# Kernel optimization log

Hardware: AMD Instinct MI355X
Metric: run time of the kernel (lower is better)

## Reference

```python
import jax, jax.numpy as jnp
import numpy as np

N_MODELS = 64
IN_F = 256
OUT_F = 256
BATCH = 8192


def setup_inputs() -> dict:
    key = jax.random.key(0)
    kx, kw, kb, ki = jax.random.split(key, 4)
    x = jax.random.normal(kx, (BATCH, OUT_F), dtype=jnp.float32)
    idxs = jax.random.randint(ki, (BATCH,), 0, N_MODELS, dtype=jnp.int64)
    # learned parameters (torch inits them to zeros; we use random so grads/outputs are nontrivial)
    w = jax.random.normal(kw, (N_MODELS, IN_F, OUT_F), dtype=jnp.float32) * 0.02
    b = jax.random.normal(kb, (N_MODELS, OUT_F), dtype=jnp.float32) * 0.02
    return {"x": x, "idxs": idxs, "w": w, "b": b}


def reference(x, idxs, w, b):
    # torch: baddbmm(b[idxs,:,None], w[idxs], x[:,:,None]).squeeze(-1) -> relu
    # y[n, i] = b[idxs[n], i] + sum_o w[idxs[n], i, o] * x[n, o]
    wg = w[idxs]                      # (B, in, out) gathered per-sample weights
    bg = b[idxs]                      # (B, out)
    y = jnp.einsum('bio,bo->bi', wg, x) + bg
    return jax.nn.relu(y)
```

## Files before the change

### kernel.cpp

```cpp
#include <hip/hip_runtime.h>
#include <stdint.h>


#define N_MODELS 64
#define IN_F     256
#define OUT_F    256
#define BATCH    8192
#define BM       128
#define BN       128

typedef __bf16 bf16x8 __attribute__((ext_vector_type(8)));
typedef float  f32x4  __attribute__((ext_vector_type(4)));
typedef __attribute__((address_space(3))) uint32_t lds_u32;
typedef const __attribute__((address_space(1))) uint32_t glb_u32;

__device__ __forceinline__ void dma16(const void* g, void* l) {
  __builtin_amdgcn_global_load_lds((glb_u32*)g, (lds_u32*)l, 16, 0, 0);
}

__device__ __forceinline__ void barrier_lds_only() {
  asm volatile("s_waitcnt lgkmcnt(0)" ::: "memory");
  __builtin_amdgcn_s_barrier();
  __builtin_amdgcn_sched_barrier(0);
}

__device__ __forceinline__ bf16x8 pack8(float4 a, float4 b) {
  bf16x8 o;
  o[0] = (__bf16)a.x; o[1] = (__bf16)a.y; o[2] = (__bf16)a.z; o[3] = (__bf16)a.w;
  o[4] = (__bf16)b.x; o[5] = (__bf16)b.y; o[6] = (__bf16)b.z; o[7] = (__bf16)b.w;
  return o;
}

__global__ __launch_bounds__(1024) void fused_kernel(
    const float* __restrict__ x, const int* __restrict__ idxs,
    const float* __restrict__ w, const float* __restrict__ bias_g,
    float* __restrict__ out) {
  const int b     = (blockIdx.x & 7) * 32 + (blockIdx.x >> 3);
  const int model = b >> 2;
  const int s     = (b >> 1) & 1;
  const int i0    = (b & 1) * BN;
  const int t     = threadIdx.x;
  const int lane  = t & 63;
  const int wv    = t >> 6;

  __shared__ float w_lds[2][BM][64];
  __shared__ float x_lds[2][BM][64];
  __shared__ int rid[BM];
  __shared__ int wsum[16];

  const float* wbase = w + (size_t)model * (IN_F * OUT_F) + (size_t)i0 * IN_F;
  const int l_r = lane >> 4;
  const int l_c = lane & 15;
#define W_DMA(q, buf)                                                        \
  {                                                                          \
    _Pragma("unroll")                                                        \
    for (int j = 0; j < 2; ++j) {                                            \
      const int r0 = wv * 8 + j * 4;                                         \
      const int rr = r0 + l_r;                                               \
      const float* gs = wbase + (size_t)rr * IN_F + (q) * 64                 \
                        + ((l_c ^ (rr & 7)) << 2);                           \
      dma16(gs, &w_lds[buf][r0][0]);                                         \
    }                                                                        \
  }

  const int4* ip = (const int4*)idxs + t * 2;
  int4 iv0 = ip[0], iv1 = ip[1];

  if (s == 0) { W_DMA(0, 0) W_DMA(1, 1) }

  if (t < BM) rid[t] = -1;

  int cnt = (iv0.x == model) + (iv0.y == model) + (iv0.z == model) + (iv0.w == model)
          + (iv1.x == model) + (iv1.y == model) + (iv1.z == model) + (iv1.w == model);
  int inc = cnt;
#pragma unroll
  for (int d = 1; d < 64; d <<= 1) {
    int u = __shfl_up(inc, d);
    if (lane >= d) inc += u;
  }
  if (lane == 63) wsum[wv] = inc;
  barrier_lds_only();
  int wpre = 0, total = 0;
#pragma unroll
  for (int j = 0; j < 16; ++j) {
    int sj = wsum[j];
    total += sj;
    if (j < wv) wpre += sj;
  }
  const int start = s * BM;
  if (start >= total) return;
  if (s == 1) { W_DMA(0, 0) W_DMA(1, 1) }

  int off = wpre + inc - cnt - start;
  {
    int n0 = t * 8;
    if (iv0.x == model) { if ((unsigned)off < BM) rid[off] = n0 + 0; ++off; }
    if (iv0.y == model) { if ((unsigned)off < BM) rid[off] = n0 + 1; ++off; }
    if (iv0.z == model) { if ((unsigned)off < BM) rid[off] = n0 + 2; ++off; }
    if (iv0.w == model) { if ((unsigned)off < BM) rid[off] = n0 + 3; ++off; }
    if (iv1.x == model) { if ((unsigned)off < BM) rid[off] = n0 + 4; ++off; }
    if (iv1.y == model) { if ((unsigned)off < BM) rid[off] = n0 + 5; ++off; }
    if (iv1.z == model) { if ((unsigned)off < BM) rid[off] = n0 + 6; ++off; }
    if (iv1.w == model) { if ((unsigned)off < BM) rid[off] = n0 + 7; ++off; }
  }
  barrier_lds_only();

  const int   r_0 = wv * 4 + l_r;
  const int   r_1 = 64 + wv * 4 + l_r;
  const int   sr0 = rid[r_0];
  const int   sr1 = rid[r_1];
  const float* xb0 = x + (size_t)(sr0 < 0 ? 0 : sr0) * IN_F
                       + ((l_c ^ (r_0 & 7)) << 2);
  const float* xb1 = x + (size_t)(sr1 < 0 ? 0 : sr1) * IN_F
                       + ((l_c ^ (r_1 & 7)) << 2);
#define X_DMA(q, buf)                                                        \
  {                                                                          \
    dma16(xb0 + (q) * 64, &x_lds[buf][wv * 4][0]);                           \
    dma16(xb1 + (q) * 64, &x_lds[buf][64 + wv * 4][0]);                      \
  }

  X_DMA(0, 0)
  X_DMA(1, 1)

  const int wm   = (wv & 3) * 32;
  const int wn   = (wv >> 2) * 32;
  const int col  = lane & 15;
  const int quad = lane >> 4;
  float bv[2];
  const float* bp = bias_g + model * OUT_F + i0 + wn + col;
#pragma unroll
  for (int nt = 0; nt < 2; ++nt) bv[nt] = bp[nt * 16];

  __syncthreads();

  f32x4 acc[2][2];
#pragma unroll
  for (int mt = 0; mt < 2; ++mt)
#pragma unroll
    for (int nt = 0; nt < 2; ++nt)
      acc[mt][nt] = (f32x4){bv[nt], bv[nt], bv[nt], bv[nt]};

#define MFMA_QUARTER(buf, ks0)                                               \
  {                                                                          \
    _Pragma("unroll")                                                        \
    for (int kk = 0; kk < 2; ++kk) {                                         \
      const int ch0 = kk * 8 + quad * 2;                                     \
      bf16x8 af[2], bfr[2];                                                  \
      _Pragma("unroll")                                                      \
      for (int mt = 0; mt < 2; ++mt) {                                       \
        const int Ra  = wm + mt * 16 + col;                                  \
        const int swa = Ra & 7;                                              \
        float4 a0 = *(const float4*)&x_lds[buf][Ra][((ch0)     ^ swa) << 2]; \
        float4 a1 = *(const float4*)&x_lds[buf][Ra][((ch0 + 1) ^ swa) << 2]; \
        af[mt] = pack8(a0, a1);                                              \
      }                                                                      \
      _Pragma("unroll")                                                      \
      for (int nt = 0; nt < 2; ++nt) {                                       \
        const int R  = wn + nt * 16 + col;                                   \
        const int sw = R & 7;                                                \
        float4 f0 = *(const float4*)&w_lds[buf][R][((ch0)     ^ sw) << 2];   \
        float4 f1 = *(const float4*)&w_lds[buf][R][((ch0 + 1) ^ sw) << 2];   \
        bfr[nt] = pack8(f0, f1);                                             \
      }                                                                      \
      _Pragma("unroll")                                                      \
      for (int mt = 0; mt < 2; ++mt)                                         \
        _Pragma("unroll")                                                    \
        for (int nt = 0; nt < 2; ++nt)                                       \
          acc[mt][nt] = __builtin_amdgcn_mfma_f32_16x16x32_bf16(             \
              af[mt], bfr[nt], acc[mt][nt], 0, 0, 0);                        \
    }                                                                        \
  }

  MFMA_QUARTER(0, 0)
  __syncthreads();
  W_DMA(2, 0) X_DMA(2, 0)
  MFMA_QUARTER(1, 2)
  __syncthreads();
  W_DMA(3, 1) X_DMA(3, 1)
  MFMA_QUARTER(0, 4)
  __syncthreads();
  MFMA_QUARTER(1, 6)

#pragma unroll
  for (int mt = 0; mt < 2; ++mt) {
#pragma unroll
    for (int reg = 0; reg < 4; ++reg) {
      const int mm = wm + mt * 16 + quad * 4 + reg;
      const int sle = rid[mm];
      if (sle >= 0) {
        float* orow = out + (size_t)sle * OUT_F + i0 + wn + col;
#pragma unroll
        for (int nt = 0; nt < 2; ++nt)
          orow[nt * 16] = fmaxf(acc[mt][nt][reg], 0.0f);
      }
    }
  }
#undef W_DMA
#undef X_DMA
#undef MFMA_QUARTER
}

extern "C" void kernel_launch(void* const* d_in, const int* in_sizes, int n_in,
                              void* d_out, int out_size, void* d_ws, size_t ws_size,
                              hipStream_t stream) {
  const float* x    = (const float*)d_in[0];
  const int*   idxs = (const int*)d_in[1];
  const float* w    = (const float*)d_in[2];
  const float* b    = (const float*)d_in[3];
  float* out = (float*)d_out;
  (void)d_ws; (void)ws_size;

  fused_kernel<<<N_MODELS * 4, 1024, 0, stream>>>(x, idxs, w, b, out);
}
```

Before: 83.70 us.

## Prefetch later K-quarters of W and X into registers and write to LDS

Quarters 2 and 3 of the weight and gathered-x tiles are now loaded into registers at kernel start, right after the DMA for quarters 0 and 1. Previously they were fetched with global_load_lds DMA only after each compute phase. After each MFMA phase the registers are written into the freed LDS buffer, so all global traffic is issued up front and later phases do not wait on fresh global latency. The later __syncthreads are replaced by an LDS-only barrier. This adds about 32 VGPRs per thread at 1024 threads per block, and an extra register-to-LDS write step.

```diff
diff --git a/kernel.cpp b/kernel.cpp
--- a/kernel.cpp
+++ b/kernel.cpp
@@ -62,11 +62,21 @@
       dma16(gs, &w_lds[buf][r0][0]);                                         \
     }                                                                        \
   }
+#define W_REG(q, dst)                                                        \
+  {                                                                          \
+    _Pragma("unroll")                                                        \
+    for (int j = 0; j < 2; ++j) {                                            \
+      const int rr = wv * 8 + j * 4 + l_r;                                   \
+      dst[j] = *(const float4*)(wbase + (size_t)rr * IN_F + (q) * 64         \
+                                + ((l_c ^ (rr & 7)) << 2));                  \
+    }                                                                        \
+  }
 
   const int4* ip = (const int4*)idxs + t * 2;
   int4 iv0 = ip[0], iv1 = ip[1];
 
-  if (s == 0) { W_DMA(0, 0) W_DMA(1, 1) }
+  float4 wr2[2], wr3[2];
+  if (s == 0) { W_DMA(0, 0) W_DMA(1, 1) W_REG(2, wr2) W_REG(3, wr3) }
 
   if (t < BM) rid[t] = -1;
 
@@ -89,7 +99,7 @@
   }
   const int start = s * BM;
   if (start >= total) return;
-  if (s == 1) { W_DMA(0, 0) W_DMA(1, 1) }
+  if (s == 1) { W_DMA(0, 0) W_DMA(1, 1) W_REG(2, wr2) W_REG(3, wr3) }
 
   int off = wpre + inc - cnt - start;
   {
@@ -121,6 +131,11 @@
 
   X_DMA(0, 0)
   X_DMA(1, 1)
+  float4 xr2[2], xr3[2];
+  xr2[0] = *(const float4*)(xb0 + 2 * 64);
+  xr2[1] = *(const float4*)(xb1 + 2 * 64);
+  xr3[0] = *(const float4*)(xb0 + 3 * 64);
+  xr3[1] = *(const float4*)(xb1 + 3 * 64);
 
   const int wm   = (wv & 3) * 32;
   const int wn   = (wv >> 2) * 32;
@@ -171,14 +186,25 @@
     }                                                                        \
   }
 
+#define WX_WRITE(buf, wreg, xreg)                                            \
+  {                                                                          \
+    _Pragma("unroll")                                                        \
+    for (int j = 0; j < 2; ++j) {                                            \
+      const int rrw = wv * 8 + j * 4 + l_r;                                  \
+      *(float4*)&w_lds[buf][rrw][l_c * 4] = wreg[j];                         \
+    }                                                                        \
+    *(float4*)&x_lds[buf][r_0][l_c * 4] = xreg[0];                           \
+    *(float4*)&x_lds[buf][r_1][l_c * 4] = xreg[1];                           \
+  }
+
   MFMA_QUARTER(0, 0)
-  __syncthreads();
-  W_DMA(2, 0) X_DMA(2, 0)
+  barrier_lds_only();
+  WX_WRITE(0, wr2, xr2)
   MFMA_QUARTER(1, 2)
-  __syncthreads();
-  W_DMA(3, 1) X_DMA(3, 1)
+  barrier_lds_only();
+  WX_WRITE(1, wr3, xr3)
   MFMA_QUARTER(0, 4)
-  __syncthreads();
+  barrier_lds_only();
   MFMA_QUARTER(1, 6)
 
 #pragma unroll
@@ -196,8 +222,10 @@
     }
   }
 #undef W_DMA
+#undef W_REG
 #undef X_DMA
 #undef MFMA_QUARTER
+#undef WX_WRITE
 }
 
 extern "C" void kernel_launch(void* const* d_in, const int* in_sizes, int n_in,
```

Result: slower. 94.72 us (+13.2%).
